# Kernel tuning notes

Measured on AMD Instinct MI355X. Metric: run time of the kernel, lower is better.

The kernel has to match this reference:

```python
import jax, jax.numpy as jnp
import numpy as np

BS = 16  # block_size

def setup_inputs() -> dict:
    key = jax.random.key(0)
    k1, k2, k3, k4, k5 = jax.random.split(key, 5)
    B, C, H, W = 4, 192, 256, 256
    x = jax.random.normal(k1, (B, C, H, W), dtype=jnp.float32)
    s = 1.0 / np.sqrt(C)
    qkv_w = jax.random.normal(k2, (3 * C, C), dtype=jnp.float32) * s
    qkv_b = jax.random.normal(k3, (3 * C,), dtype=jnp.float32) * 0.01
    proj_w = jax.random.normal(k4, (C, C), dtype=jnp.float32) * s
    proj_b = jax.random.normal(k5, (C,), dtype=jnp.float32) * 0.01
    return {"x": x, "qkv_w": qkv_w, "qkv_b": qkv_b, "proj_w": proj_w, "proj_b": proj_b}

def reference(x, qkv_w, qkv_b, proj_w, proj_b):
    B, C, H, W = x.shape
    nh, nw = H // BS, W // BS
    N = BS * BS  # tokens per window
    # [B,C,H,W] -> [B*nh*nw, C, N]  (windowing, matches torch unfold/unfold)
    xb = x.reshape(B, C, nh, BS, nw, BS).transpose(0, 2, 4, 1, 3, 5)
    xb = xb.reshape(B * nh * nw, C, N)
    # 1x1-conv QKV projection as a GEMM over channels
    qkv = jnp.einsum('oc,bcn->bon', qkv_w, xb) + qkv_b[None, :, None]  # [Bb,3C,N]
    q, k, v = jnp.split(qkv, 3, axis=1)  # each [Bb, C, N]
    # attention: softmax(q^T k) over last dim (no scaling, as in original)
    att = jax.nn.softmax(jnp.einsum('bcn,bcm->bnm', q, k), axis=-1)  # [Bb,N,N]
    out = jnp.einsum('bnm,bcm->bcn', att, v)  # [Bb, C, N]
    # un-window back to [B, C, H, W]
    y = out.reshape(B, nh, nw, C, BS, BS).transpose(0, 3, 1, 4, 2, 5)
    y = y.reshape(B, C, H, W)
    # 1x1-conv output projection + residual
    proj = jnp.einsum('oc,bchw->bohw', proj_w, y) + proj_b[None, :, None, None]
    return proj + x
```

## Files before the change

### kernel.cpp

```cpp
#include <hip/hip_runtime.h>
#include <stdint.h>

typedef _Float16 f16;
typedef __attribute__((ext_vector_type(8))) _Float16 f16x8;
typedef __attribute__((ext_vector_type(4))) float f32x4;

#define MFMA(a, b, c) __builtin_amdgcn_mfma_f32_16x16x32_f16((a), (b), (c), 0, 0, 0)

static constexpr int C = 192;

union U8x { uint2 u2[2]; f16x8 v; };

__global__ __launch_bounds__(256)
void prep_kernel(const float* __restrict__ qkv_w, const float* __restrict__ qkv_b,
                 const float* __restrict__ proj_w, const float* __restrict__ proj_b,
                 f16* __restrict__ Mh, f16* __restrict__ Wo, float* __restrict__ b2) {
    const int idx = blockIdx.x * 256 + threadIdx.x;
    if (idx < 256 * 192) {
        const int r = idx / 192, c = idx % 192;
        float s = 0.f;
        if (r < 192) {
#pragma unroll 4
            for (int o = 0; o < 192; ++o)
                s += qkv_w[o * 192 + r] * qkv_w[(192 + o) * 192 + c];
        } else if (r == 192) {
#pragma unroll 4
            for (int o = 0; o < 192; ++o)
                s += qkv_b[o] * qkv_w[(192 + o) * 192 + c];
        }
        Mh[idx] = (f16)s;
    } else if (idx < 256 * 192 + 192 * 192) {
        const int j = idx - 256 * 192;
        const int r = j / 192, c = j % 192;
        float s = 0.f;
#pragma unroll 4
        for (int c2 = 0; c2 < 192; ++c2)
            s += proj_w[r * 192 + c2] * qkv_w[(384 + c2) * 192 + c];
        Wo[j] = (f16)s;
    } else if (idx < 256 * 192 + 192 * 192 + 192) {
        const int o = idx - (256 * 192 + 192 * 192);
        float s = proj_b[o];
        for (int c2 = 0; c2 < 192; ++c2)
            s += proj_w[o * 192 + c2] * qkv_b[384 + c2];
        b2[o] = s;
    }
}

#define XS 200
__global__ __launch_bounds__(256, 4)
void xt_kernel(const float* __restrict__ x, const f16* __restrict__ Mh,
               f16* __restrict__ tpk, f16* __restrict__ xh) {
    __shared__ f16 xs[64 * XS];
    const int tid = threadIdx.x;
    const int wg = blockIdx.x;
    const int win = wg >> 2, tb = wg & 3;
    const int batch = win >> 8, wh = (win >> 4) & 15, ww = win & 15;
    const int i0 = tb * 4;

    for (int e = 0; e < 12; ++e) {
        int f = e * 1024 + tid * 4;
        int c = f >> 6, nl = f & 63;
        int i = nl >> 4, j = nl & 15;
        const float4 v4 = *(const float4*)(x + (((size_t)(batch * C + c) * 256 + (wh * 16 + i0 + i)) * 256 + ww * 16 + j));
        xs[(nl + 0) * XS + c] = (f16)v4.x;
        xs[(nl + 1) * XS + c] = (f16)v4.y;
        xs[(nl + 2) * XS + c] = (f16)v4.z;
        xs[(nl + 3) * XS + c] = (f16)v4.w;
    }
    __syncthreads();

    const int wave = tid >> 6, lane = tid & 63, l15 = lane & 15, qd = lane >> 4;
    const int rb = wave;
    const int nmi = (wave == 3) ? 1 : 4;
    f32x4 acc[4][4] = {};
#pragma unroll
    for (int k = 0; k < 6; ++k) {
        const int c0 = k * 32 + qd * 8;
        f16x8 af[4], bf[4];
#pragma unroll
        for (int mi = 0; mi < 4; ++mi)
            if (mi < nmi)
                af[mi] = *(const f16x8*)(Mh + (rb * 64 + mi * 16 + l15) * C + c0);
#pragma unroll
        for (int ti = 0; ti < 4; ++ti)
            bf[ti] = *(const f16x8*)(xs + (ti * 16 + l15) * XS + c0);
#pragma unroll
        for (int mi = 0; mi < 4; ++mi)
            if (mi < nmi)
#pragma unroll
                for (int ti = 0; ti < 4; ++ti)
                    acc[mi][ti] = MFMA(af[mi], bf[ti], acc[mi][ti]);
    }
#pragma unroll
    for (int mi = 0; mi < 4; ++mi) {
        if (mi >= nmi) continue;
        const int c4 = rb * 16 + mi * 4 + qd;
        if (c4 < 49) {
#pragma unroll
            for (int ti = 0; ti < 4; ++ti) {
                const int tok = tb * 64 + ti * 16 + l15;
                union { f16 h[4]; uint2 u; } pk;
                pk.h[0] = (f16)acc[mi][ti][0];
                pk.h[1] = (f16)acc[mi][ti][1];
                pk.h[2] = (f16)acc[mi][ti][2];
                pk.h[3] = (f16)acc[mi][ti][3];
                *(uint2*)(tpk + (((size_t)win * 49 + c4) * 256 + tok) * 4) = pk.u;
            }
        }
    }
    for (int it = 0; it < 12; ++it) {
        int e = it * 256 + tid;
        int c = e >> 4, t4 = (e & 15) * 4;
        union { f16 h[4]; uint2 u; } pk;
        pk.h[0] = xs[(t4 + 0) * XS + c];
        pk.h[1] = xs[(t4 + 1) * XS + c];
        pk.h[2] = xs[(t4 + 2) * XS + c];
        pk.h[3] = xs[(t4 + 3) * XS + c];
        *(uint2*)(xh + ((size_t)win * C + c) * 256 + tb * 64 + t4) = pk.u;
    }
}

#define SQS 200
#define SPS 72
__global__ __launch_bounds__(256, 4)
void attn_kernel(const float* __restrict__ x, const f16* __restrict__ tpk,
                 const f16* __restrict__ xh, const f16* __restrict__ Wo,
                 const float* __restrict__ b2, float* __restrict__ out) {
    __shared__ f16 sQ[64 * SQS];
    __shared__ f16 sP[64 * SPS];
    __shared__ float sRed[4][64];
    __shared__ float sMax[64];
    __shared__ float sSum[64];

    const int tid = threadIdx.x;
    const int wg = blockIdx.x;
    const int win = ((wg >> 5) << 3) | (wg & 7);
    const int rblk = (wg >> 3) & 3;
    const int batch = win >> 8, wh = (win >> 4) & 15, ww = win & 15;
    const int wave = tid >> 6, lane = tid & 63, l15 = lane & 15, qd = lane >> 4;

    for (int e = 0; e < 12; ++e) {
        int f = e * 1024 + tid * 4;
        int c = f >> 6, nl = f & 63;
        int i = nl >> 4, j = nl & 15;
        const float4 v4 = *(const float4*)(x + (((size_t)(batch * C + c) * 256 + (wh * 16 + rblk * 4 + i)) * 256 + ww * 16 + j));
        sQ[(nl + 0) * SQS + c] = (f16)v4.x;
        sQ[(nl + 1) * SQS + c] = (f16)v4.y;
        sQ[(nl + 2) * SQS + c] = (f16)v4.z;
        sQ[(nl + 3) * SQS + c] = (f16)v4.w;
    }
    float vm[4];
#pragma unroll
    for (int ti = 0; ti < 4; ++ti)
        vm[ti] = (float)tpk[(((size_t)win * 49 + 48) * 256 + wave * 64 + ti * 16 + l15) * 4];
    __syncthreads();

    f32x4 accS[4][4] = {};
#pragma unroll
    for (int k = 0; k < 6; ++k) {
        const int c0 = k * 32 + qd * 8;
        const int c4 = c0 >> 2;
        f16x8 af[4], bf[4];
#pragma unroll
        for (int mi = 0; mi < 4; ++mi)
            af[mi] = *(const f16x8*)(sQ + (mi * 16 + l15) * SQS + c0);
#pragma unroll
        for (int ti = 0; ti < 4; ++ti) {
            const int m = wave * 64 + ti * 16 + l15;
            const size_t a = (((size_t)win * 49 + c4) * 256 + m) * 4;
            U8x b;
            b.u2[0] = *(const uint2*)(tpk + a);
            b.u2[1] = *(const uint2*)(tpk + a + 1024);
            bf[ti] = b.v;
        }
#pragma unroll
        for (int mi = 0; mi < 4; ++mi)
#pragma unroll
            for (int ti = 0; ti < 4; ++ti)
                accS[mi][ti] = MFMA(af[mi], bf[ti], accS[mi][ti]);
    }
#pragma unroll
    for (int mi = 0; mi < 4; ++mi)
#pragma unroll
        for (int ti = 0; ti < 4; ++ti)
#pragma unroll
            for (int r = 0; r < 4; ++r)
                accS[mi][ti][r] += vm[ti];

    float pm[4][4];
#pragma unroll
    for (int mi = 0; mi < 4; ++mi)
#pragma unroll
        for (int r = 0; r < 4; ++r) {
            float m = fmaxf(fmaxf(accS[mi][0][r], accS[mi][1][r]),
                            fmaxf(accS[mi][2][r], accS[mi][3][r]));
#pragma unroll
            for (int d = 1; d < 16; d <<= 1) m = fmaxf(m, __shfl_xor(m, d, 64));
            pm[mi][r] = m;
        }
    if (l15 == 0) {
#pragma unroll
        for (int mi = 0; mi < 4; ++mi)
#pragma unroll
            for (int r = 0; r < 4; ++r) sRed[wave][mi * 16 + qd * 4 + r] = pm[mi][r];
    }
    __syncthreads();
    if (tid < 64)
        sMax[tid] = fmaxf(fmaxf(sRed[0][tid], sRed[1][tid]), fmaxf(sRed[2][tid], sRed[3][tid]));
    __syncthreads();

    union PK { f16 h[4]; uint2 u; };
    PK pH[4][4];
    float ps[4][4];
#pragma unroll
    for (int mi = 0; mi < 4; ++mi)
#pragma unroll
        for (int r = 0; r < 4; ++r) {
            const float M = sMax[mi * 16 + qd * 4 + r];
            float s = 0.f;
#pragma unroll
            for (int ti = 0; ti < 4; ++ti) {
                float e = __expf(accS[mi][ti][r] - M);
                pH[mi][ti].h[r] = (f16)e;
                s += e;
            }
#pragma unroll
            for (int d = 1; d < 16; d <<= 1) s += __shfl_xor(s, d, 64);
            ps[mi][r] = s;
        }
    if (l15 == 0) {
#pragma unroll
        for (int mi = 0; mi < 4; ++mi)
#pragma unroll
            for (int r = 0; r < 4; ++r) sRed[wave][mi * 16 + qd * 4 + r] = ps[mi][r];
    }
    __syncthreads();
    if (tid < 64) sSum[tid] = sRed[0][tid] + sRed[1][tid] + sRed[2][tid] + sRed[3][tid];

    f32x4 accO[4][3] = {};
#pragma unroll
    for (int h = 0; h < 4; ++h) {
        if (wave == h) {
#pragma unroll
            for (int mi = 0; mi < 4; ++mi)
#pragma unroll
                for (int ti = 0; ti < 4; ++ti)
#pragma unroll
                    for (int r = 0; r < 4; ++r)
                        sP[(mi * 16 + qd * 4 + r) * SPS + ti * 16 + l15] = pH[mi][ti].h[r];
        }
        __syncthreads();
#pragma unroll
        for (int k = 0; k < 2; ++k) {
            const int ml = k * 32 + qd * 8;
            const int m0 = h * 64 + ml;
            f16x8 af[4], bf[3];
#pragma unroll
            for (int tn = 0; tn < 4; ++tn)
                af[tn] = *(const f16x8*)(sP + (tn * 16 + l15) * SPS + ml);
#pragma unroll
            for (int tc = 0; tc < 3; ++tc)
                bf[tc] = *(const f16x8*)(xh + ((size_t)win * C + wave * 48 + tc * 16 + l15) * 256 + m0);
#pragma unroll
            for (int tn = 0; tn < 4; ++tn)
#pragma unroll
                for (int tc = 0; tc < 3; ++tc)
                    accO[tn][tc] = MFMA(af[tn], bf[tc], accO[tn][tc]);
        }
        if (h < 3) __syncthreads();
    }

    f16* sOT = sQ;
#pragma unroll
    for (int tn = 0; tn < 4; ++tn)
#pragma unroll
        for (int r = 0; r < 4; ++r) {
            const int n = tn * 16 + qd * 4 + r;
            const float rs = 1.0f / sSum[n];
#pragma unroll
            for (int tc = 0; tc < 3; ++tc)
                sOT[n * SQS + wave * 48 + tc * 16 + l15] = (f16)(accO[tn][tc][r] * rs);
        }
    __syncthreads();

    f32x4 accP[3][4] = {};
#pragma unroll
    for (int k = 0; k < 6; ++k) {
        const int c0 = k * 32 + qd * 8;
        f16x8 af[3], bf[4];
#pragma unroll
        for (int to = 0; to < 3; ++to)
            af[to] = *(const f16x8*)(Wo + (wave * 48 + to * 16 + l15) * C + c0);
#pragma unroll
        for (int tn = 0; tn < 4; ++tn)
            bf[tn] = *(const f16x8*)(sOT + (tn * 16 + l15) * SQS + c0);
#pragma unroll
        for (int to = 0; to < 3; ++to)
#pragma unroll
            for (int tn = 0; tn < 4; ++tn)
                accP[to][tn] = MFMA(af[to], bf[tn], accP[to][tn]);
    }
#pragma unroll
    for (int to = 0; to < 3; ++to)
#pragma unroll
        for (int r = 0; r < 4; ++r) {
            const int o = wave * 48 + to * 16 + qd * 4 + r;
            const float pb = b2[o];
#pragma unroll
            for (int tn = 0; tn < 4; ++tn) {
                const size_t idx = (((size_t)(batch * C + o) * 256) + wh * 16 + rblk * 4 + tn) * 256 + ww * 16 + l15;
                out[idx] = accP[to][tn][r] + pb + x[idx];
            }
        }
}

extern "C" void kernel_launch(void* const* d_in, const int* in_sizes, int n_in,
                              void* d_out, int out_size, void* d_ws, size_t ws_size,
                              hipStream_t stream) {
    const float* x      = (const float*)d_in[0];
    const float* qkv_w  = (const float*)d_in[1];
    const float* qkv_b  = (const float*)d_in[2];
    const float* proj_w = (const float*)d_in[3];
    const float* proj_b = (const float*)d_in[4];
    float* out = (float*)d_out;

    char* ws = (char*)d_ws;
    const size_t TPK_BYTES = (size_t)1024 * 49 * 256 * 4 * 2;
    const size_t XH_BYTES  = (size_t)1024 * 192 * 256 * 2;
    const size_t MH_BYTES  = (size_t)256 * 192 * 2;
    const size_t WO_BYTES  = (size_t)192 * 192 * 2;
    f16*   tpk = (f16*)(ws);
    f16*   xh  = (f16*)(ws + TPK_BYTES);
    f16*   Mh  = (f16*)(ws + TPK_BYTES + XH_BYTES);
    f16*   Wo  = (f16*)(ws + TPK_BYTES + XH_BYTES + MH_BYTES);
    float* b2  = (float*)(ws + TPK_BYTES + XH_BYTES + MH_BYTES + WO_BYTES);

    prep_kernel<<<337, 256, 0, stream>>>(qkv_w, qkv_b, proj_w, proj_b, Mh, Wo, b2);
    xt_kernel<<<4096, 256, 0, stream>>>(x, Mh, tpk, xh);
    attn_kernel<<<4096, 256, 0, stream>>>(x, tpk, xh, Wo, b2, out);
}
```

Measured before the change: 790.6 us.

## Pre-pack f16 query tile in xt_kernel and halve P·V barrier rounds

xt_kernel now also writes an f16 packed copy of the window (xq) and the separate vm row (vmg), so attn_kernel loads its Q tile as f16 chunks instead of re-reading and converting fp32 x with a strided transpose. The P·V loop stages two waves' probabilities at once (wider sP buffer, two rounds instead of four), cutting synchronisations. The residual x values are prefetched into registers before the output projection. This costs an extra f16 workspace write/read, more shared memory and registers, and occupancy drops from 4 to 3 blocks per CU.

```diff
diff --git a/kernel.cpp b/kernel.cpp
--- a/kernel.cpp
+++ b/kernel.cpp
@@ -49,7 +49,8 @@
 #define XS 200
 __global__ __launch_bounds__(256, 4)
 void xt_kernel(const float* __restrict__ x, const f16* __restrict__ Mh,
-               f16* __restrict__ tpk, f16* __restrict__ xh) {
+               f16* __restrict__ tpk, f16* __restrict__ vmg,
+               f16* __restrict__ xq, f16* __restrict__ xh) {
     __shared__ f16 xs[64 * XS];
     const int tid = threadIdx.x;
     const int wg = blockIdx.x;
@@ -69,44 +70,11 @@
     }
     __syncthreads();
 
-    const int wave = tid >> 6, lane = tid & 63, l15 = lane & 15, qd = lane >> 4;
-    const int rb = wave;
-    const int nmi = (wave == 3) ? 1 : 4;
-    f32x4 acc[4][4] = {};
-#pragma unroll
-    for (int k = 0; k < 6; ++k) {
-        const int c0 = k * 32 + qd * 8;
-        f16x8 af[4], bf[4];
-#pragma unroll
-        for (int mi = 0; mi < 4; ++mi)
-            if (mi < nmi)
-                af[mi] = *(const f16x8*)(Mh + (rb * 64 + mi * 16 + l15) * C + c0);
-#pragma unroll
-        for (int ti = 0; ti < 4; ++ti)
-            bf[ti] = *(const f16x8*)(xs + (ti * 16 + l15) * XS + c0);
-#pragma unroll
-        for (int mi = 0; mi < 4; ++mi)
-            if (mi < nmi)
-#pragma unroll
-                for (int ti = 0; ti < 4; ++ti)
-                    acc[mi][ti] = MFMA(af[mi], bf[ti], acc[mi][ti]);
-    }
-#pragma unroll
-    for (int mi = 0; mi < 4; ++mi) {
-        if (mi >= nmi) continue;
-        const int c4 = rb * 16 + mi * 4 + qd;
-        if (c4 < 49) {
-#pragma unroll
-            for (int ti = 0; ti < 4; ++ti) {
-                const int tok = tb * 64 + ti * 16 + l15;
-                union { f16 h[4]; uint2 u; } pk;
-                pk.h[0] = (f16)acc[mi][ti][0];
-                pk.h[1] = (f16)acc[mi][ti][1];
-                pk.h[2] = (f16)acc[mi][ti][2];
-                pk.h[3] = (f16)acc[mi][ti][3];
-                *(uint2*)(tpk + (((size_t)win * 49 + c4) * 256 + tok) * 4) = pk.u;
-            }
-        }
+    for (int it = 0; it < 12; ++it) {
+        int e = it * 256 + tid;
+        int n = e & 63, c4 = e >> 6;
+        *(uint2*)(xq + (((size_t)win * 48 + c4) * 256 + tb * 64 + n) * 4) =
+            *(const uint2*)(xs + n * XS + c4 * 4);
     }
     for (int it = 0; it < 12; ++it) {
         int e = it * 256 + tid;
@@ -118,14 +86,58 @@
         pk.h[3] = xs[(t4 + 3) * XS + c];
         *(uint2*)(xh + ((size_t)win * C + c) * 256 + tb * 64 + t4) = pk.u;
     }
+
+    const int wave = tid >> 6, lane = tid & 63, l15 = lane & 15, qd = lane >> 4;
+    const int rb = wave;
+    const int nmi = (wave == 3) ? 1 : 4;
+    f32x4 acc[4][4] = {};
+#pragma unroll
+    for (int k = 0; k < 6; ++k) {
+        const int c0 = k * 32 + qd * 8;
+        f16x8 af[4], bf[4];
+#pragma unroll
+        for (int mi = 0; mi < 4; ++mi)
+            if (mi < nmi)
+                af[mi] = *(const f16x8*)(Mh + (rb * 64 + mi * 16 + l15) * C + c0);
+#pragma unroll
+        for (int ti = 0; ti < 4; ++ti)
+            bf[ti] = *(const f16x8*)(xs + (ti * 16 + l15) * XS + c0);
+#pragma unroll
+        for (int mi = 0; mi < 4; ++mi)
+            if (mi < nmi)
+#pragma unroll
+                for (int ti = 0; ti < 4; ++ti)
+                    acc[mi][ti] = MFMA(af[mi], bf[ti], acc[mi][ti]);
+    }
+    if (rb < 3) {
+#pragma unroll
+        for (int mi = 0; mi < 4; ++mi) {
+            const int c4 = rb * 16 + mi * 4 + qd;
+#pragma unroll
+            for (int ti = 0; ti < 4; ++ti) {
+                const int tok = tb * 64 + ti * 16 + l15;
+                union { f16 h[4]; uint2 u; } pk;
+                pk.h[0] = (f16)acc[mi][ti][0];
+                pk.h[1] = (f16)acc[mi][ti][1];
+                pk.h[2] = (f16)acc[mi][ti][2];
+                pk.h[3] = (f16)acc[mi][ti][3];
+                *(uint2*)(tpk + (((size_t)win * 48 + c4) * 256 + tok) * 4) = pk.u;
+            }
+        }
+    } else if (qd == 0) {
+#pragma unroll
+        for (int ti = 0; ti < 4; ++ti)
+            vmg[(size_t)win * 256 + tb * 64 + ti * 16 + l15] = (f16)acc[0][ti][0];
+    }
 }
 
 #define SQS 200
-#define SPS 72
-__global__ __launch_bounds__(256, 4)
-void attn_kernel(const float* __restrict__ x, const f16* __restrict__ tpk,
-                 const f16* __restrict__ xh, const f16* __restrict__ Wo,
-                 const float* __restrict__ b2, float* __restrict__ out) {
+#define SPS 136
+__global__ __launch_bounds__(256, 3)
+void attn_kernel(const f16* __restrict__ xq, const f16* __restrict__ tpk,
+                 const f16* __restrict__ vmg, const f16* __restrict__ xh,
+                 const f16* __restrict__ Wo, const float* __restrict__ b2,
+                 const float* __restrict__ x, float* __restrict__ out) {
     __shared__ f16 sQ[64 * SQS];
     __shared__ f16 sP[64 * SPS];
     __shared__ float sRed[4][64];
@@ -136,23 +148,20 @@
     const int wg = blockIdx.x;
     const int win = ((wg >> 5) << 3) | (wg & 7);
     const int rblk = (wg >> 3) & 3;
+    const int n0 = rblk * 64;
     const int batch = win >> 8, wh = (win >> 4) & 15, ww = win & 15;
     const int wave = tid >> 6, lane = tid & 63, l15 = lane & 15, qd = lane >> 4;
 
-    for (int e = 0; e < 12; ++e) {
-        int f = e * 1024 + tid * 4;
-        int c = f >> 6, nl = f & 63;
-        int i = nl >> 4, j = nl & 15;
-        const float4 v4 = *(const float4*)(x + (((size_t)(batch * C + c) * 256 + (wh * 16 + rblk * 4 + i)) * 256 + ww * 16 + j));
-        sQ[(nl + 0) * SQS + c] = (f16)v4.x;
-        sQ[(nl + 1) * SQS + c] = (f16)v4.y;
-        sQ[(nl + 2) * SQS + c] = (f16)v4.z;
-        sQ[(nl + 3) * SQS + c] = (f16)v4.w;
+    for (int it = 0; it < 12; ++it) {
+        int ch = it * 256 + tid;
+        int n = ch & 63, c4 = ch >> 6;
+        *(uint2*)(sQ + n * SQS + c4 * 4) =
+            *(const uint2*)(xq + (((size_t)win * 48 + c4) * 256 + n0 + n) * 4);
     }
     float vm[4];
 #pragma unroll
     for (int ti = 0; ti < 4; ++ti)
-        vm[ti] = (float)tpk[(((size_t)win * 49 + 48) * 256 + wave * 64 + ti * 16 + l15) * 4];
+        vm[ti] = (float)vmg[(size_t)win * 256 + wave * 64 + ti * 16 + l15];
     __syncthreads();
 
     f32x4 accS[4][4] = {};
@@ -167,7 +176,7 @@
 #pragma unroll
         for (int ti = 0; ti < 4; ++ti) {
             const int m = wave * 64 + ti * 16 + l15;
-            const size_t a = (((size_t)win * 49 + c4) * 256 + m) * 4;
+            const size_t a = (((size_t)win * 48 + c4) * 256 + m) * 4;
             U8x b;
             b.u2[0] = *(const uint2*)(tpk + a);
             b.u2[1] = *(const uint2*)(tpk + a + 1024);
@@ -239,21 +248,22 @@
 
     f32x4 accO[4][3] = {};
 #pragma unroll
-    for (int h = 0; h < 4; ++h) {
-        if (wave == h) {
+    for (int h = 0; h < 2; ++h) {
+        if ((wave >> 1) == h) {
+            const int cl = (wave & 1) * 64;
 #pragma unroll
             for (int mi = 0; mi < 4; ++mi)
 #pragma unroll
                 for (int ti = 0; ti < 4; ++ti)
 #pragma unroll
                     for (int r = 0; r < 4; ++r)
-                        sP[(mi * 16 + qd * 4 + r) * SPS + ti * 16 + l15] = pH[mi][ti].h[r];
+                        sP[(mi * 16 + qd * 4 + r) * SPS + cl + ti * 16 + l15] = pH[mi][ti].h[r];
         }
         __syncthreads();
 #pragma unroll
-        for (int k = 0; k < 2; ++k) {
+        for (int k = 0; k < 4; ++k) {
             const int ml = k * 32 + qd * 8;
-            const int m0 = h * 64 + ml;
+            const int m0 = h * 128 + ml;
             f16x8 af[4], bf[3];
 #pragma unroll
             for (int tn = 0; tn < 4; ++tn)
@@ -267,8 +277,21 @@
                 for (int tc = 0; tc < 3; ++tc)
                     accO[tn][tc] = MFMA(af[tn], bf[tc], accO[tn][tc]);
         }
-        if (h < 3) __syncthreads();
-    }
+        if (h == 0) __syncthreads();
+    }
+
+    float xres[3][4][4];
+#pragma unroll
+    for (int to = 0; to < 3; ++to)
+#pragma unroll
+        for (int r = 0; r < 4; ++r) {
+            const int o = wave * 48 + to * 16 + qd * 4 + r;
+#pragma unroll
+            for (int tn = 0; tn < 4; ++tn) {
+                const size_t idx = (((size_t)(batch * C + o) * 256) + wh * 16 + rblk * 4 + tn) * 256 + ww * 16 + l15;
+                xres[to][r][tn] = x[idx];
+            }
+        }
 
     f16* sOT = sQ;
 #pragma unroll
@@ -309,7 +332,7 @@
 #pragma unroll
             for (int tn = 0; tn < 4; ++tn) {
                 const size_t idx = (((size_t)(batch * C + o) * 256) + wh * 16 + rblk * 4 + tn) * 256 + ww * 16 + l15;
-                out[idx] = accP[to][tn][r] + pb + x[idx];
+                out[idx] = accP[to][tn][r] + pb + xres[to][r][tn];
             }
         }
 }
@@ -325,17 +348,17 @@
     float* out = (float*)d_out;
 
     char* ws = (char*)d_ws;
-    const size_t TPK_BYTES = (size_t)1024 * 49 * 256 * 4 * 2;
-    const size_t XH_BYTES  = (size_t)1024 * 192 * 256 * 2;
-    const size_t MH_BYTES  = (size_t)256 * 192 * 2;
-    const size_t WO_BYTES  = (size_t)192 * 192 * 2;
+    const size_t PK_BYTES  = (size_t)1024 * 48 * 256 * 4 * 2;
+    const size_t VMG_BYTES = (size_t)1024 * 256 * 2;
     f16*   tpk = (f16*)(ws);
-    f16*   xh  = (f16*)(ws + TPK_BYTES);
-    f16*   Mh  = (f16*)(ws + TPK_BYTES + XH_BYTES);
-    f16*   Wo  = (f16*)(ws + TPK_BYTES + XH_BYTES + MH_BYTES);
-    float* b2  = (float*)(ws + TPK_BYTES + XH_BYTES + MH_BYTES + WO_BYTES);
+    f16*   xq  = (f16*)(ws + PK_BYTES);
+    f16*   xh  = (f16*)(ws + 2 * PK_BYTES);
+    f16*   vmg = (f16*)(ws + 3 * PK_BYTES);
+    f16*   Mh  = (f16*)(ws + 3 * PK_BYTES + VMG_BYTES);
+    f16*   Wo  = (f16*)(ws + 3 * PK_BYTES + VMG_BYTES + 256 * 192 * 2);
+    float* b2  = (float*)(ws + 3 * PK_BYTES + VMG_BYTES + 256 * 192 * 2 + 192 * 192 * 2);
 
     prep_kernel<<<337, 256, 0, stream>>>(qkv_w, qkv_b, proj_w, proj_b, Mh, Wo, b2);
-    xt_kernel<<<4096, 256, 0, stream>>>(x, Mh, tpk, xh);
-    attn_kernel<<<4096, 256, 0, stream>>>(x, tpk, xh, Wo, b2, out);
+    xt_kernel<<<4096, 256, 0, stream>>>(x, Mh, tpk, vmg, xq, xh);
+    attn_kernel<<<4096, 256, 0, stream>>>(xq, tpk, vmg, xh, Wo, b2, x, out);
 }
```

New measurement: 649.6 us. 1.22x faster.
